# Kernel optimization log

Measured on AMD Instinct MI355X. Metric: run time of the kernel, lower is better.

## Reference

```python
import jax, jax.numpy as jnp
import numpy as np

B, C, H, W = 512, 256, 7, 7
NS, HS, WS = 16, 14, 14
CK = 128            # key/value channels of the 1x1 convs
REP = 1024          # MLP_HEAD_DIM
IN = 2 * CK * H * W # 12544 = concat(query_value, attended_value) flattened


def setup_inputs() -> dict:
    key = jax.random.key(0)
    ks = jax.random.split(key, 14)
    s = lambda n: 1.0 / np.sqrt(n)
    f32 = jnp.float32
    return {
        "x": jax.random.normal(ks[0], (B, C, H, W), f32),
        "sup_features": jax.random.normal(ks[1], (NS, C, HS, WS), f32),
        # 1x1 conv weights [out_c, in_c] + biases
        "Wqv": jax.random.normal(ks[2], (CK, C), f32) * s(C),
        "bqv": jnp.zeros((CK,), f32),
        "Wqk": jax.random.normal(ks[3], (CK, C), f32) * s(C),
        "bqk": jnp.zeros((CK,), f32),
        "Wsv": jax.random.normal(ks[4], (CK, C), f32) * s(C),
        "bsv": jnp.zeros((CK,), f32),
        "Wsk": jax.random.normal(ks[5], (CK, C), f32) * s(C),
        "bsk": jnp.zeros((CK,), f32),
        # fc layers, torch Linear convention: W [out, in]
        "W6c": jax.random.normal(ks[6], (REP, IN), f32) * s(IN),
        "b6c": jnp.zeros((REP,), f32),
        "W7c": jax.random.normal(ks[7], (REP, REP), f32) * s(REP),
        "b7c": jnp.zeros((REP,), f32),
        "W6r": jax.random.normal(ks[8], (REP, IN), f32) * s(IN),
        "b6r": jnp.zeros((REP,), f32),
        "W7r": jax.random.normal(ks[9], (REP, REP), f32) * s(REP),
        "b7r": jnp.zeros((REP,), f32),
    }


def _conv1x1(w, b, t):
    # 1x1 conv == per-pixel channel mixing
    return jnp.einsum('oc,bchw->bohw', w, t) + b[None, :, None, None]


def reference(x, sup_features, Wqv, bqv, Wqk, bqk, Wsv, bsv, Wsk, bsk,
              W6c, b6c, W7c, b7c, W6r, b6r, W7r, b7r):
    qv = _conv1x1(Wqv, bqv, x)                                          # [B,128,H,W]
    qk = _conv1x1(Wqk, bqk, x).transpose(0, 2, 3, 1).reshape(-1, CK)    # [B*H*W,128]
    sv = _conv1x1(Wsv, bsv, sup_features).transpose(0, 2, 3, 1).reshape(-1, CK)  # [M,128]
    sk = _conv1x1(Wsk, bsk, sup_features).transpose(1, 0, 2, 3).reshape(CK, -1)  # [128,M]
    sim = jax.nn.softmax(qk @ sk, axis=-1)                              # [B*H*W, M] (unscaled, as in source)
    att = (sim @ sv).reshape(B, H, W, CK).transpose(0, 3, 1, 2)         # [B,128,H,W]
    fuse = jnp.concatenate([qv, att], axis=1).reshape(B, -1)            # [B,12544]
    xr = jax.nn.relu(fuse @ W6r.T + b6r)
    xr = jax.nn.relu(xr @ W7r.T + b7r)
    xc = jax.nn.relu(fuse @ W6c.T + b6c)
    xc = jax.nn.relu(xc @ W7c.T + b7c)
    return (xc, xr)
```

## Files before the change

kernel.cpp:

```cpp
#include <hip/hip_runtime.h>
#include <hip/hip_bf16.h>
#include <stdint.h>

typedef short short8 __attribute__((ext_vector_type(8)));
typedef float f32x4 __attribute__((ext_vector_type(4)));
typedef ushort ushort4v __attribute__((ext_vector_type(4)));

#define M_Q   25088
#define M_S   3136
#define IN_   12544
#define LOG2E  1.44269504f
#define SHIFT2 57.7078016f
#define NZ    8
#define FZ    8
#define KSTR  136
#define PSTR  40
#define WSTR  40

__device__ __forceinline__ ushort f2bf(float f) {
  union { float f; uint32_t u; } v; v.f = f;
  uint32_t r = v.u + 0x7fffu + ((v.u >> 16) & 1u);
  return (ushort)(r >> 16);
}
__device__ __forceinline__ ushort f2bf_fast(float f) {
  union { float f; uint32_t u; } v; v.f = f;
  return (ushort)((v.u + 0x8000u) >> 16);
}
__device__ __forceinline__ float bf2f(ushort u) {
  union { uint32_t u; float f; } v; v.u = ((uint32_t)u) << 16;
  return v.f;
}
__device__ __forceinline__ f32x4 mfma16(short8 a, short8 b, f32x4 c) {
  return __builtin_amdgcn_mfma_f32_16x16x32_bf16(a, b, c, 0, 0, 0);
}

__global__ void pack_w(const float* __restrict__ Wqv, const float* __restrict__ Wqk,
                       const float* __restrict__ bqv, const float* __restrict__ bqk,
                       const float* __restrict__ Wsv, const float* __restrict__ Wsk,
                       const float* __restrict__ bsv, const float* __restrict__ bsk,
                       ushort* __restrict__ Wq_h, float* __restrict__ biasq,
                       ushort* __restrict__ Ws_h, float* __restrict__ biass) {
  int idx = blockIdx.x * 256 + threadIdx.x;
  if (idx < 65536) {
    int n = idx >> 8;
    const float* W = (n < 128) ? (Wqv + n * 256) : (Wqk + (n - 128) * 256);
    Wq_h[idx] = f2bf(W[idx & 255]);
  } else if (idx < 131072) {
    int j = idx - 65536;
    int n = j >> 8;
    const float* W = (n < 128) ? (Wsv + n * 256) : (Wsk + (n - 128) * 256);
    Ws_h[j] = f2bf(W[j & 255]);
  } else if (idx < 131328) {
    int n = idx - 131072;
    biasq[n] = (n < 128) ? bqv[n] : bqk[n - 128];
  } else if (idx < 131584) {
    int n = idx - 131328;
    biass[n] = (n < 128) ? bsv[n] : bsk[n - 128];
  }
}

__global__ __launch_bounds__(256) void pack_w6(
    const float* __restrict__ W6c, const float* __restrict__ W6r,
    ushort* __restrict__ W6p) {
  __shared__ ushort tile[IN_];
  const int n = blockIdx.x;
  const float* src = (n < 1024) ? (W6c + (size_t)n * IN_)
                                : (W6r + (size_t)(n - 1024) * IN_);
  ushort* dst = W6p + (size_t)n * IN_;
#pragma unroll 7
  for (int j = 0; j < 49; ++j) {
    int i = j * 256 + threadIdx.x;
    tile[i] = f2bf(src[i]);
  }
  __syncthreads();
#pragma unroll 7
  for (int j = 0; j < 49; ++j) {
    int o = j * 256 + threadIdx.x;
    int c = o & 255, p = o >> 8;
    dst[o] = tile[c * 49 + p];
  }
}

__global__ void pack_w7(const float* __restrict__ W7c, const float* __restrict__ W7r,
                        ushort* __restrict__ W7p) {
  int idx = blockIdx.x * 256 + threadIdx.x;
  float v = (idx < 1048576) ? W7c[idx] : W7r[idx - 1048576];
  W7p[idx] = f2bf(v);
}

__global__ __launch_bounds__(256) void gemm_conv_q(
    const float* __restrict__ x, const ushort* __restrict__ Bh,
    const float* __restrict__ bias, ushort* __restrict__ fuse,
    ushort* __restrict__ qk_h) {
  const int lane = threadIdx.x & 63, wv = threadIdx.x >> 6;
  const int r = lane & 15, g = lane >> 4;
  const int row0 = blockIdx.x * 64 + wv * 16;
  const int q = row0 + r;
  const int b = q / 49, p = q - b * 49;
  const float* xb = x + (size_t)b * IN_ + p;
  f32x4 acc[16];
#pragma unroll
  for (int i = 0; i < 16; ++i) acc[i] = f32x4{0.f, 0.f, 0.f, 0.f};
#pragma unroll
  for (int kc = 0; kc < 8; ++kc) {
    const float* s = xb + (size_t)(kc * 32 + g * 8) * 49;
    short8 ah;
#pragma unroll
    for (int j = 0; j < 8; ++j) ah[j] = (short)f2bf(s[(size_t)j * 49]);
    const ushort* bbh = Bh + r * 256 + kc * 32 + g * 8;
#pragma unroll
    for (int nt = 0; nt < 16; ++nt) {
      short8 bh = *(const short8*)(bbh + nt * 16 * 256);
      acc[nt] = mfma16(ah, bh, acc[nt]);
    }
  }
  const int qr = row0 + g * 4;
#pragma unroll
  for (int nt = 0; nt < 16; ++nt) {
    int n = nt * 16 + r;
    float bs = bias[n];
#pragma unroll
    for (int e = 0; e < 4; ++e) {
      float v = acc[nt][e] + bs;
      int qq = qr + e;
      if (nt < 8) {
        int bb = qq / 49, pp = qq - bb * 49;
        fuse[(size_t)bb * IN_ + pp * 256 + n] = f2bf(v);
      } else {
        qk_h[(size_t)qq * 128 + (n - 128)] = f2bf(v * LOG2E);
      }
    }
  }
}

__global__ __launch_bounds__(256) void gemm_conv_s(
    const float* __restrict__ sup, const ushort* __restrict__ Bh,
    const float* __restrict__ bias, ushort* __restrict__ svT,
    ushort* __restrict__ sk_h) {
  const int lane = threadIdx.x & 63, wv = threadIdx.x >> 6;
  const int r = lane & 15, g = lane >> 4;
  const int row0 = blockIdx.x * 64 + wv * 16;
  const int nb = blockIdx.y;
  const int q = row0 + r;
  const int b = q / 196, p = q - b * 196;
  const float* xb = sup + (size_t)b * 256 * 196 + p;
  f32x4 acc[8];
#pragma unroll
  for (int i = 0; i < 8; ++i) acc[i] = f32x4{0.f, 0.f, 0.f, 0.f};
#pragma unroll
  for (int kc = 0; kc < 8; ++kc) {
    const float* s = xb + (size_t)(kc * 32 + g * 8) * 196;
    short8 ah;
#pragma unroll
    for (int j = 0; j < 8; ++j) ah[j] = (short)f2bf(s[(size_t)j * 196]);
    const ushort* bbh = Bh + (size_t)(nb * 128 + r) * 256 + kc * 32 + g * 8;
#pragma unroll
    for (int nt = 0; nt < 8; ++nt) {
      short8 bh = *(const short8*)(bbh + nt * 16 * 256);
      acc[nt] = mfma16(ah, bh, acc[nt]);
    }
  }
  const int qr = row0 + g * 4;
#pragma unroll
  for (int nt = 0; nt < 8; ++nt) {
    int nl = nt * 16 + r;
    float bs = bias[nb * 128 + nl];
#pragma unroll
    for (int e = 0; e < 4; ++e) {
      float v = acc[nt][e] + bs;
      int k = qr + e;
      if (nb == 0) {
        svT[(size_t)nl * M_S + k] = f2bf(v);
      } else {
        sk_h[(size_t)k * 128 + nl] = f2bf(v);
      }
    }
  }
}

#define LOAD_TILE(T)                                                            \
  do {                                                                          \
    const int kb_ = (T) * 32;                                                   \
    pkh0 = *(const short8*)(Kh + (size_t)(kb_ + row0s) * 128 + c8s * 8);        \
    pkh1 = *(const short8*)(Kh + (size_t)(kb_ + row0s + 16) * 128 + c8s * 8);   \
    pv0  = *(const short8*)(Vt + (size_t)cvs * M_S + kb_ + kc2s * 8);           \
    pv1  = *(const short8*)(Vt + (size_t)(cvs + 64) * M_S + kb_ + kc2s * 8);    \
  } while (0)
#define PUBLISH(B)                                                              \
  do {                                                                          \
    *(short8*)(&khs[B][kloff0]) = pkh0;                                         \
    *(short8*)(&khs[B][kloff1]) = pkh1;                                         \
    *(short8*)(&vvs[B][voff0]) = pv0;                                           \
    *(short8*)(&vvs[B][voff1]) = pv1;                                           \
  } while (0)

__global__ __launch_bounds__(256) void attn_kernel(
    const ushort* __restrict__ Qh, const ushort* __restrict__ Kh,
    const ushort* __restrict__ Vt, ushort* __restrict__ pnum,
    float* __restrict__ pden) {
  __shared__ ushort khs[2][32 * KSTR];
  __shared__ ushort vvs[2][128 * 32];
  __shared__ ushort plds[4][16 * PSTR];
  const int tid = threadIdx.x;
  const int w = tid >> 6, lane = tid & 63;
  const int r = lane & 15, g = lane >> 4;
  const int q0 = blockIdx.x * 128 + w * 32;
  const int z = blockIdx.y;
  const int t0 = z * 12 + (z < 2 ? z : 2);
  const int tn = 12 + (z < 2 ? 1 : 0);
  ushort* pw = plds[w];

  const int row0s = tid >> 4, c8s = tid & 15;
  const int cvs = tid >> 2, kc2s = tid & 3;
  const int kloff0 = row0s * KSTR + c8s * 8;
  const int kloff1 = (row0s + 16) * KSTR + c8s * 8;
  const int voff0 = cvs * 32 + kc2s * 8;
  const int voff1 = (cvs + 64) * 32 + kc2s * 8;

  short8 aq[2][4];
#pragma unroll
  for (int mt = 0; mt < 2; ++mt)
#pragma unroll
    for (int kc = 0; kc < 4; ++kc)
      aq[mt][kc] = *(const short8*)(Qh + (size_t)(q0 + mt * 16 + r) * 128 + kc * 32 + g * 8);

  f32x4 acc[2][8];
#pragma unroll
  for (int mt = 0; mt < 2; ++mt)
#pragma unroll
    for (int ct = 0; ct < 8; ++ct) acc[mt][ct] = f32x4{0.f, 0.f, 0.f, 0.f};
  float den[2][4];
#pragma unroll
  for (int mt = 0; mt < 2; ++mt)
#pragma unroll
    for (int e = 0; e < 4; ++e) den[mt][e] = 0.f;

  short8 pkh0, pkh1, pv0, pv1;
  LOAD_TILE(t0);
  PUBLISH(0);
  if (tn > 1) LOAD_TILE(t0 + 1);
  __syncthreads();

  for (int i = 0; i < tn; ++i) {
    const int b = i & 1;
    if (i + 1 < tn) {
      PUBLISH(b ^ 1);
      if (i + 2 < tn) LOAD_TILE(t0 + i + 2);
    }
    f32x4 lg[2][2];
#pragma unroll
    for (int kt = 0; kt < 2; ++kt) {
      const int kbase = (kt * 16 + r) * KSTR;
      short8 bh[4];
#pragma unroll
      for (int kc = 0; kc < 4; ++kc)
        bh[kc] = *(const short8*)(&khs[b][kbase + (kc * 4 + g) * 8]);
#pragma unroll
      for (int mt = 0; mt < 2; ++mt) {
        f32x4 c = f32x4{0.f, 0.f, 0.f, 0.f};
#pragma unroll
        for (int kc = 0; kc < 4; ++kc)
          c = mfma16(aq[mt][kc], bh[kc], c);
        lg[mt][kt] = c;
      }
    }
    short8 vf[8];
#pragma unroll
    for (int ct = 0; ct < 8; ++ct)
      vf[ct] = *(const short8*)(&vvs[b][(ct * 16 + r) * 32 + g * 8]);
#pragma unroll
    for (int mt = 0; mt < 2; ++mt) {
#pragma unroll
      for (int kt = 0; kt < 2; ++kt)
#pragma unroll
        for (int e = 0; e < 4; ++e) {
          float p = __builtin_amdgcn_exp2f(lg[mt][kt][e] - SHIFT2);
          den[mt][e] += p;
          pw[(g * 4 + e) * PSTR + kt * 16 + r] = f2bf_fast(p);
        }
      short8 pf = *(const short8*)(pw + r * PSTR + g * 8);
#pragma unroll
      for (int ct = 0; ct < 8; ++ct)
        acc[mt][ct] = mfma16(pf, vf[ct], acc[mt][ct]);
    }
    __syncthreads();
  }

#pragma unroll
  for (int mt = 0; mt < 2; ++mt)
#pragma unroll
    for (int e = 0; e < 4; ++e) {
      float d = den[mt][e];
      d += __shfl_xor(d, 1);
      d += __shfl_xor(d, 2);
      d += __shfl_xor(d, 4);
      d += __shfl_xor(d, 8);
      den[mt][e] = d;
    }
#pragma unroll
  for (int mt = 0; mt < 2; ++mt)
#pragma unroll
    for (int ct = 0; ct < 8; ++ct)
#pragma unroll
      for (int e = 0; e < 4; ++e) {
        int q = q0 + mt * 16 + g * 4 + e;
        int c = ct * 16 + r;
        pnum[((size_t)z * M_Q + q) * 128 + c] = f2bf_fast(acc[mt][ct][e]);
      }
  if (r == 0) {
#pragma unroll
    for (int mt = 0; mt < 2; ++mt)
#pragma unroll
      for (int e = 0; e < 4; ++e)
        pden[(size_t)z * M_Q + q0 + mt * 16 + g * 4 + e] = den[mt][e];
  }
}

__global__ void attn_reduce(const ushort* __restrict__ pnum, const float* __restrict__ pden,
                            ushort* __restrict__ fuse) {
  int idx = blockIdx.x * 256 + threadIdx.x;
  int q = idx >> 5;
  int c4 = (idx & 31) * 4;
  float4 s = {0.f, 0.f, 0.f, 0.f};
  float d = 0.f;
#pragma unroll
  for (int z = 0; z < NZ; ++z) {
    ushort4v v = *(const ushort4v*)(pnum + ((size_t)z * M_Q + q) * 128 + c4);
    s.x += bf2f(v[0]); s.y += bf2f(v[1]); s.z += bf2f(v[2]); s.w += bf2f(v[3]);
    d += pden[(size_t)z * M_Q + q];
  }
  float inv = 1.0f / d;
  int b = q / 49, p = q - b * 49;
  ushort4v o;
  o[0] = f2bf(s.x * inv); o[1] = f2bf(s.y * inv);
  o[2] = f2bf(s.z * inv); o[3] = f2bf(s.w * inv);
  *(ushort4v*)(fuse + (size_t)b * IN_ + p * 256 + 128 + c4) = o;
}

__global__ __launch_bounds__(256) void fc6_kernel(
    const ushort* __restrict__ fuse, const ushort* __restrict__ W6p,
    float* __restrict__ part) {
  __shared__ ushort wlds[2][64 * WSTR];
  const int lane = threadIdx.x & 63, wv = threadIdx.x >> 6;
  const int r = lane & 15, g = lane >> 4;
  const int m0 = wv * 128;
  const int kz = blockIdx.x & 7;
  const int nidx = (blockIdx.x >> 3) + 4 * blockIdx.y;
  const int n0 = nidx * 64;
  const int k0 = kz * 1568;

  const int srow = threadIdx.x >> 2;
  const int skc  = (threadIdx.x & 3) * 8;
  const size_t wgbase = (size_t)(n0 + srow) * IN_ + k0 + skc;
  const int wloff = srow * WSTR + skc;

  f32x4 acc[8][4];
#pragma unroll
  for (int mt = 0; mt < 8; ++mt)
#pragma unroll
    for (int nt = 0; nt < 4; ++nt) acc[mt][nt] = f32x4{0.f, 0.f, 0.f, 0.f};

  short8 rA, rB;
  rA = *(const short8*)(W6p + wgbase);
  *(short8*)(&wlds[0][wloff]) = rA;
  rA = *(const short8*)(W6p + wgbase + 32);
  rB = *(const short8*)(W6p + wgbase + 64);
  __syncthreads();

  for (int t = 0; t < 49; ++t) {
    const int b = t & 1;
    if (t + 1 < 49) {
      *(short8*)(&wlds[b ^ 1][wloff]) = rA;
      rA = rB;
      if (t + 3 < 49) rB = *(const short8*)(W6p + wgbase + (size_t)(t + 3) * 32);
    }
    const int kcol = k0 + t * 32 + g * 8;
    short8 af[8];
#pragma unroll
    for (int mt = 0; mt < 8; ++mt)
      af[mt] = *(const short8*)(fuse + (size_t)(m0 + mt * 16 + r) * IN_ + kcol);
    short8 bfr[4];
#pragma unroll
    for (int nt = 0; nt < 4; ++nt)
      bfr[nt] = *(const short8*)(&wlds[b][(nt * 16 + r) * WSTR + g * 8]);
#pragma unroll
    for (int mt = 0; mt < 8; ++mt)
#pragma unroll
      for (int nt = 0; nt < 4; ++nt) acc[mt][nt] = mfma16(af[mt], bfr[nt], acc[mt][nt]);
    __syncthreads();
  }
#pragma unroll
  for (int mt = 0; mt < 8; ++mt)
#pragma unroll
    for (int nt = 0; nt < 4; ++nt)
#pragma unroll
      for (int e = 0; e < 4; ++e) {
        int m = m0 + mt * 16 + g * 4 + e;
        int n = n0 + nt * 16 + r;
        part[(size_t)kz * 1048576 + (size_t)m * 2048 + n] = acc[mt][nt][e];
      }
}

__global__ void fc6_reduce(const float* __restrict__ part, const float* __restrict__ b6c,
                           const float* __restrict__ b6r, ushort* __restrict__ X7) {
  int idx = blockIdx.x * 256 + threadIdx.x;
  int n = idx & 2047;
  float s = 0.f;
#pragma unroll
  for (int z = 0; z < FZ; ++z) s += part[(size_t)z * 1048576 + idx];
  s += (n < 1024) ? b6c[n] : b6r[n - 1024];
  s = fmaxf(s, 0.f);
  X7[idx] = f2bf(s);
}

__global__ __launch_bounds__(128) void fc7_kernel(
    const ushort* __restrict__ X7, const ushort* __restrict__ W7p,
    const float* __restrict__ b7c, const float* __restrict__ b7r,
    float* __restrict__ out) {
  const int lane = threadIdx.x & 63, wv = threadIdx.x >> 6;
  const int r = lane & 15, g = lane >> 4;
  const int m0 = blockIdx.x * 32 + wv * 16;
  const int n0 = blockIdx.y * 32;
  const int half = (n0 >= 1024) ? 1 : 0;
  const int nn0 = n0 - half * 1024;
  const float* b7 = half ? b7r : b7c;
  f32x4 acc[2];
#pragma unroll
  for (int nt = 0; nt < 2; ++nt) acc[nt] = f32x4{0.f, 0.f, 0.f, 0.f};
  const ushort* arow = X7 + (size_t)(m0 + r) * 2048 + half * 1024;
  for (int kk = 0; kk < 1024; kk += 32) {
    short8 a = *(const short8*)(arow + kk + g * 8);
#pragma unroll
    for (int nt = 0; nt < 2; ++nt) {
      short8 bb = *(const short8*)(W7p + (size_t)(half * 1024 + nn0 + nt * 16 + r) * 1024 + kk + g * 8);
      acc[nt] = mfma16(a, bb, acc[nt]);
    }
  }
  float* obase = out + (size_t)half * 524288;
#pragma unroll
  for (int nt = 0; nt < 2; ++nt) {
#pragma unroll
    for (int e = 0; e < 4; ++e) {
      int m = m0 + g * 4 + e;
      int n = nn0 + nt * 16 + r;
      obase[(size_t)m * 1024 + n] = fmaxf(acc[nt][e] + b7[n], 0.f);
    }
  }
}

extern "C" void kernel_launch(void* const* d_in, const int* in_sizes, int n_in,
                              void* d_out, int out_size, void* d_ws, size_t ws_size,
                              hipStream_t stream) {
  const float* x    = (const float*)d_in[0];
  const float* sup  = (const float*)d_in[1];
  const float* Wqv  = (const float*)d_in[2];
  const float* bqv  = (const float*)d_in[3];
  const float* Wqk  = (const float*)d_in[4];
  const float* bqk  = (const float*)d_in[5];
  const float* Wsv  = (const float*)d_in[6];
  const float* bsv  = (const float*)d_in[7];
  const float* Wsk  = (const float*)d_in[8];
  const float* bsk  = (const float*)d_in[9];
  const float* W6c  = (const float*)d_in[10];
  const float* b6c  = (const float*)d_in[11];
  const float* W7c  = (const float*)d_in[12];
  const float* b7c  = (const float*)d_in[13];
  const float* W6r  = (const float*)d_in[14];
  const float* b6r  = (const float*)d_in[15];
  const float* W7r  = (const float*)d_in[16];
  const float* b7r  = (const float*)d_in[17];
  float* out = (float*)d_out;

  char* base = (char*)d_ws;
  size_t off = 0;
  auto alloc = [&](size_t bytes) {
    char* p = base + off;
    off += (bytes + 255) & ~(size_t)255;
    return p;
  };
  char* regionB = alloc((size_t)NZ * M_Q * 128 * 2);
  ushort* pnum = (ushort*)regionB;
  float*  part = (float*)regionB;
  ushort* W6p  = (ushort*)alloc((size_t)2048 * IN_ * 2);
  ushort* W7p  = (ushort*)alloc((size_t)2048 * 1024 * 2);
  ushort* Wq_h = (ushort*)alloc(65536 * 2);
  ushort* Ws_h = (ushort*)alloc(65536 * 2);
  float*  biasq = (float*)alloc(256 * 4);
  float*  biass = (float*)alloc(256 * 4);
  ushort* fuse = (ushort*)alloc((size_t)512 * IN_ * 2);
  ushort* qk_h = (ushort*)alloc((size_t)M_Q * 128 * 2);
  ushort* sk_h = (ushort*)alloc((size_t)M_S * 128 * 2);
  ushort* svT  = (ushort*)alloc((size_t)M_S * 128 * 2);
  float*  pden = (float*)alloc((size_t)NZ * M_Q * 4);
  ushort* X7   = (ushort*)alloc((size_t)512 * 2048 * 2);
  if (off > ws_size) return;

  pack_w<<<dim3(515), dim3(256), 0, stream>>>(Wqv, Wqk, bqv, bqk, Wsv, Wsk, bsv, bsk,
                                              Wq_h, biasq, Ws_h, biass);
  pack_w6<<<dim3(2048), dim3(256), 0, stream>>>(W6c, W6r, W6p);
  pack_w7<<<dim3(8192), dim3(256), 0, stream>>>(W7c, W7r, W7p);
  gemm_conv_q<<<dim3(392), dim3(256), 0, stream>>>(x, Wq_h, biasq, fuse, qk_h);
  gemm_conv_s<<<dim3(49, 2), dim3(256), 0, stream>>>(sup, Ws_h, biass, svT, sk_h);
  attn_kernel<<<dim3(196, NZ), dim3(256), 0, stream>>>(qk_h, sk_h, svT, pnum, pden);
  attn_reduce<<<dim3(3136), dim3(256), 0, stream>>>(pnum, pden, fuse);
  fc6_kernel<<<dim3(32, FZ), dim3(256), 0, stream>>>(fuse, W6p, part);
  fc6_reduce<<<dim3(4096), dim3(256), 0, stream>>>(part, b6c, b6r, X7);
  fc7_kernel<<<dim3(16, 64), dim3(128), 0, stream>>>(X7, W7p, b7c, b7r, out);
}
```

Baseline: 274.7 us.

## Merge weight-pack kernels, add MFMA priority hints, widen fc6 blocks to 512 threads

Merges the three weight-packing kernels into one launch, dispatching on block index, to cut launch overhead. Wraps the attention kernel's MFMA sections in s_setprio so waves in matrix work get issue priority. Doubles fc6 block size to 8 waves, each handling 64 rows instead of 128, with only the first 256 threads staging weights; this halves accumulator registers per wave and raises parallelism, at the cost of more LDS readers per staged tile. The packing kernel's 24KB shared tile now applies to every block, including the simple W7 and small-weight blocks.

Result: faster. 252.1 us (-8.2%).

```diff
diff --git a/kernel.cpp b/kernel.cpp
--- a/kernel.cpp
+++ b/kernel.cpp
@@ -34,58 +34,59 @@
   return __builtin_amdgcn_mfma_f32_16x16x32_bf16(a, b, c, 0, 0, 0);
 }
 
-__global__ void pack_w(const float* __restrict__ Wqv, const float* __restrict__ Wqk,
-                       const float* __restrict__ bqv, const float* __restrict__ bqk,
-                       const float* __restrict__ Wsv, const float* __restrict__ Wsk,
-                       const float* __restrict__ bsv, const float* __restrict__ bsk,
-                       ushort* __restrict__ Wq_h, float* __restrict__ biasq,
-                       ushort* __restrict__ Ws_h, float* __restrict__ biass) {
-  int idx = blockIdx.x * 256 + threadIdx.x;
-  if (idx < 65536) {
-    int n = idx >> 8;
-    const float* W = (n < 128) ? (Wqv + n * 256) : (Wqk + (n - 128) * 256);
-    Wq_h[idx] = f2bf(W[idx & 255]);
-  } else if (idx < 131072) {
-    int j = idx - 65536;
-    int n = j >> 8;
-    const float* W = (n < 128) ? (Wsv + n * 256) : (Wsk + (n - 128) * 256);
-    Ws_h[j] = f2bf(W[j & 255]);
-  } else if (idx < 131328) {
-    int n = idx - 131072;
-    biasq[n] = (n < 128) ? bqv[n] : bqk[n - 128];
-  } else if (idx < 131584) {
-    int n = idx - 131328;
-    biass[n] = (n < 128) ? bsv[n] : bsk[n - 128];
-  }
-}
-
-__global__ __launch_bounds__(256) void pack_w6(
+__global__ __launch_bounds__(256) void pack_all(
     const float* __restrict__ W6c, const float* __restrict__ W6r,
-    ushort* __restrict__ W6p) {
+    ushort* __restrict__ W6p,
+    const float* __restrict__ W7c, const float* __restrict__ W7r,
+    ushort* __restrict__ W7p,
+    const float* __restrict__ Wqv, const float* __restrict__ Wqk,
+    const float* __restrict__ bqv, const float* __restrict__ bqk,
+    const float* __restrict__ Wsv, const float* __restrict__ Wsk,
+    const float* __restrict__ bsv, const float* __restrict__ bsk,
+    ushort* __restrict__ Wq_h, float* __restrict__ biasq,
+    ushort* __restrict__ Ws_h, float* __restrict__ biass) {
   __shared__ ushort tile[IN_];
-  const int n = blockIdx.x;
-  const float* src = (n < 1024) ? (W6c + (size_t)n * IN_)
-                                : (W6r + (size_t)(n - 1024) * IN_);
-  ushort* dst = W6p + (size_t)n * IN_;
+  const int bid = blockIdx.x;
+  if (bid < 2048) {
+    const int n = bid;
+    const float* src = (n < 1024) ? (W6c + (size_t)n * IN_)
+                                  : (W6r + (size_t)(n - 1024) * IN_);
+    ushort* dst = W6p + (size_t)n * IN_;
 #pragma unroll 7
-  for (int j = 0; j < 49; ++j) {
-    int i = j * 256 + threadIdx.x;
-    tile[i] = f2bf(src[i]);
-  }
-  __syncthreads();
+    for (int j = 0; j < 49; ++j) {
+      int i = j * 256 + threadIdx.x;
+      tile[i] = f2bf(src[i]);
+    }
+    __syncthreads();
 #pragma unroll 7
-  for (int j = 0; j < 49; ++j) {
-    int o = j * 256 + threadIdx.x;
-    int c = o & 255, p = o >> 8;
-    dst[o] = tile[c * 49 + p];
-  }
-}
-
-__global__ void pack_w7(const float* __restrict__ W7c, const float* __restrict__ W7r,
-                        ushort* __restrict__ W7p) {
-  int idx = blockIdx.x * 256 + threadIdx.x;
-  float v = (idx < 1048576) ? W7c[idx] : W7r[idx - 1048576];
-  W7p[idx] = f2bf(v);
+    for (int j = 0; j < 49; ++j) {
+      int o = j * 256 + threadIdx.x;
+      int c = o & 255, p = o >> 8;
+      dst[o] = tile[c * 49 + p];
+    }
+  } else if (bid < 10240) {
+    int idx = (bid - 2048) * 256 + threadIdx.x;
+    float v = (idx < 1048576) ? W7c[idx] : W7r[idx - 1048576];
+    W7p[idx] = f2bf(v);
+  } else {
+    int idx = (bid - 10240) * 256 + threadIdx.x;
+    if (idx < 65536) {
+      int n = idx >> 8;
+      const float* W = (n < 128) ? (Wqv + n * 256) : (Wqk + (n - 128) * 256);
+      Wq_h[idx] = f2bf(W[idx & 255]);
+    } else if (idx < 131072) {
+      int j = idx - 65536;
+      int n = j >> 8;
+      const float* W = (n < 128) ? (Wsv + n * 256) : (Wsk + (n - 128) * 256);
+      Ws_h[j] = f2bf(W[j & 255]);
+    } else if (idx < 131328) {
+      int n = idx - 131072;
+      biasq[n] = (n < 128) ? bqv[n] : bqk[n - 128];
+    } else if (idx < 131584) {
+      int n = idx - 131328;
+      biass[n] = (n < 128) ? bsv[n] : bsk[n - 128];
+    }
+  }
 }
 
 __global__ __launch_bounds__(256) void gemm_conv_q(
@@ -248,6 +249,7 @@
       if (i + 2 < tn) LOAD_TILE(t0 + i + 2);
     }
     f32x4 lg[2][2];
+    __builtin_amdgcn_s_setprio(1);
 #pragma unroll
     for (int kt = 0; kt < 2; ++kt) {
       const int kbase = (kt * 16 + r) * KSTR;
@@ -264,6 +266,7 @@
         lg[mt][kt] = c;
       }
     }
+    __builtin_amdgcn_s_setprio(0);
     short8 vf[8];
 #pragma unroll
     for (int ct = 0; ct < 8; ++ct)
@@ -279,9 +282,11 @@
           pw[(g * 4 + e) * PSTR + kt * 16 + r] = f2bf_fast(p);
         }
       short8 pf = *(const short8*)(pw + r * PSTR + g * 8);
+      __builtin_amdgcn_s_setprio(1);
 #pragma unroll
       for (int ct = 0; ct < 8; ++ct)
         acc[mt][ct] = mfma16(pf, vf[ct], acc[mt][ct]);
+      __builtin_amdgcn_s_setprio(0);
     }
     __syncthreads();
   }
@@ -337,13 +342,13 @@
   *(ushort4v*)(fuse + (size_t)b * IN_ + p * 256 + 128 + c4) = o;
 }
 
-__global__ __launch_bounds__(256) void fc6_kernel(
+__global__ __launch_bounds__(512) void fc6_kernel(
     const ushort* __restrict__ fuse, const ushort* __restrict__ W6p,
     float* __restrict__ part) {
   __shared__ ushort wlds[2][64 * WSTR];
   const int lane = threadIdx.x & 63, wv = threadIdx.x >> 6;
   const int r = lane & 15, g = lane >> 4;
-  const int m0 = wv * 128;
+  const int m0 = wv * 64;
   const int kz = blockIdx.x & 7;
   const int nidx = (blockIdx.x >> 3) + 4 * blockIdx.y;
   const int n0 = nidx * 64;
@@ -351,46 +356,49 @@
 
   const int srow = threadIdx.x >> 2;
   const int skc  = (threadIdx.x & 3) * 8;
-  const size_t wgbase = (size_t)(n0 + srow) * IN_ + k0 + skc;
-  const int wloff = srow * WSTR + skc;
-
-  f32x4 acc[8][4];
-#pragma unroll
-  for (int mt = 0; mt < 8; ++mt)
+  const bool stager = (threadIdx.x < 256);
+  const size_t wgbase = (size_t)(n0 + (srow & 63)) * IN_ + k0 + skc;
+  const int wloff = (srow & 63) * WSTR + skc;
+
+  f32x4 acc[4][4];
+#pragma unroll
+  for (int mt = 0; mt < 4; ++mt)
 #pragma unroll
     for (int nt = 0; nt < 4; ++nt) acc[mt][nt] = f32x4{0.f, 0.f, 0.f, 0.f};
 
   short8 rA, rB;
-  rA = *(const short8*)(W6p + wgbase);
-  *(short8*)(&wlds[0][wloff]) = rA;
-  rA = *(const short8*)(W6p + wgbase + 32);
-  rB = *(const short8*)(W6p + wgbase + 64);
+  if (stager) {
+    rA = *(const short8*)(W6p + wgbase);
+    *(short8*)(&wlds[0][wloff]) = rA;
+    rA = *(const short8*)(W6p + wgbase + 32);
+    rB = *(const short8*)(W6p + wgbase + 64);
+  }
   __syncthreads();
 
   for (int t = 0; t < 49; ++t) {
     const int b = t & 1;
-    if (t + 1 < 49) {
+    if (t + 1 < 49 && stager) {
       *(short8*)(&wlds[b ^ 1][wloff]) = rA;
       rA = rB;
       if (t + 3 < 49) rB = *(const short8*)(W6p + wgbase + (size_t)(t + 3) * 32);
     }
     const int kcol = k0 + t * 32 + g * 8;
-    short8 af[8];
-#pragma unroll
-    for (int mt = 0; mt < 8; ++mt)
+    short8 af[4];
+#pragma unroll
+    for (int mt = 0; mt < 4; ++mt)
       af[mt] = *(const short8*)(fuse + (size_t)(m0 + mt * 16 + r) * IN_ + kcol);
     short8 bfr[4];
 #pragma unroll
     for (int nt = 0; nt < 4; ++nt)
       bfr[nt] = *(const short8*)(&wlds[b][(nt * 16 + r) * WSTR + g * 8]);
 #pragma unroll
-    for (int mt = 0; mt < 8; ++mt)
+    for (int mt = 0; mt < 4; ++mt)
 #pragma unroll
       for (int nt = 0; nt < 4; ++nt) acc[mt][nt] = mfma16(af[mt], bfr[nt], acc[mt][nt]);
     __syncthreads();
   }
 #pragma unroll
-  for (int mt = 0; mt < 8; ++mt)
+  for (int mt = 0; mt < 4; ++mt)
 #pragma unroll
     for (int nt = 0; nt < 4; ++nt)
 #pragma unroll
@@ -495,15 +503,14 @@
   ushort* X7   = (ushort*)alloc((size_t)512 * 2048 * 2);
   if (off > ws_size) return;
 
-  pack_w<<<dim3(515), dim3(256), 0, stream>>>(Wqv, Wqk, bqv, bqk, Wsv, Wsk, bsv, bsk,
-                                              Wq_h, biasq, Ws_h, biass);
-  pack_w6<<<dim3(2048), dim3(256), 0, stream>>>(W6c, W6r, W6p);
-  pack_w7<<<dim3(8192), dim3(256), 0, stream>>>(W7c, W7r, W7p);
+  pack_all<<<dim3(10755), dim3(256), 0, stream>>>(W6c, W6r, W6p, W7c, W7r, W7p,
+                                                  Wqv, Wqk, bqv, bqk, Wsv, Wsk,
+                                                  bsv, bsk, Wq_h, biasq, Ws_h, biass);
   gemm_conv_q<<<dim3(392), dim3(256), 0, stream>>>(x, Wq_h, biasq, fuse, qk_h);
   gemm_conv_s<<<dim3(49, 2), dim3(256), 0, stream>>>(sup, Ws_h, biass, svT, sk_h);
   attn_kernel<<<dim3(196, NZ), dim3(256), 0, stream>>>(qk_h, sk_h, svT, pnum, pden);
   attn_reduce<<<dim3(3136), dim3(256), 0, stream>>>(pnum, pden, fuse);
-  fc6_kernel<<<dim3(32, FZ), dim3(256), 0, stream>>>(fuse, W6p, part);
+  fc6_kernel<<<dim3(32, FZ), dim3(512), 0, stream>>>(fuse, W6p, part);
   fc6_reduce<<<dim3(4096), dim3(256), 0, stream>>>(part, b6c, b6r, X7);
   fc7_kernel<<<dim3(16, 64), dim3(128), 0, stream>>>(X7, W7p, b7c, b7r, out);
 }
```
